# Kernel optimization log

Hardware: AMD Instinct MI355X
Metric: run time of the kernel (lower is better)

## Reference

```python
import jax, jax.numpy as jnp
import numpy as np

# Poincare ball, curvature c = 1.0 (manifold.c)
C = 1.0
SQC = 1.0  # sqrt(C)
EPS = 1e-15
BALL_EPS = 1e-5
ALPHA = 0.1  # params[0]


def _project(x):
    # clip points back inside the open ball
    norm = jnp.linalg.norm(x, axis=-1, keepdims=True)
    maxnorm = (1.0 - BALL_EPS) / SQC
    return jnp.where(norm > maxnorm, x / jnp.maximum(norm, EPS) * maxnorm, x)


def _artanh(x):
    return jnp.arctanh(jnp.clip(x, -1.0 + 1e-7, 1.0 - 1e-7))


def _lambda_x(x):
    # conformal factor lambda_x = 2 / (1 - c||x||^2)
    return 2.0 / jnp.maximum(1.0 - C * jnp.sum(x * x, axis=-1, keepdims=True), EPS)


def _mobius_scalar_mul(r, x):
    n = jnp.maximum(jnp.linalg.norm(x, axis=-1, keepdims=True), EPS)
    return jnp.tanh(r * _artanh(SQC * n)) * x / (SQC * n)


def _mobius_add(x, y):
    x2 = jnp.sum(x * x, axis=-1, keepdims=True)
    y2 = jnp.sum(y * y, axis=-1, keepdims=True)
    xy = jnp.sum(x * y, axis=-1, keepdims=True)
    num = (1.0 + 2.0 * C * xy + C * y2) * x + (1.0 - C * x2) * y
    den = 1.0 + 2.0 * C * xy + C * C * x2 * y2
    return num / jnp.maximum(den, EPS)


def _expmap0(u):
    n = jnp.maximum(jnp.linalg.norm(u, axis=-1, keepdims=True), EPS)
    return jnp.tanh(SQC * n) * u / (SQC * n)


def _mobius_matvec(W, x):
    # Mobius matrix-vector multiply: expmap0-style rescale of x @ W^T
    xn = jnp.maximum(jnp.linalg.norm(x, axis=-1, keepdims=True), EPS)
    mx = x @ W.T
    mxn = jnp.maximum(jnp.linalg.norm(mx, axis=-1, keepdims=True), EPS)
    res = jnp.tanh(mxn / xn * _artanh(SQC * xn)) * mx / (SQC * mxn)
    return _project(res)


def _clamp_abs(x, eps=1e-10):
    return jnp.where(x >= 0, jnp.maximum(x, eps), jnp.minimum(x, -eps))


def weighted_midpoint_spmm(x, src, dst, w, n):
    # gyro-midpoint of neighbors under sparse adjacency weights
    gamma = _lambda_x(x)                                   # [N,1]
    msg = (gamma * x)[src] * w[:, None]                    # [E,d] irregular gather
    num = jax.ops.segment_sum(msg, dst, num_segments=n)    # [N,d]
    den = jax.ops.segment_sum(jnp.abs(w) * (gamma[:, 0] - 1.0)[src], dst,
                              num_segments=n)[:, None]     # [N,1]
    return _project(_mobius_scalar_mul(0.5, num / _clamp_abs(den)))


def weighted_midpoint_pair(a, b, wa, wb):
    # weighted_midpoint(stack([a,b],dim=1), weights=[wa,wb], reducedim=[1])
    ga, gb = _lambda_x(a), _lambda_x(b)
    num = wa * ga * a + wb * gb * b
    den = abs(wa) * (ga - 1.0) + abs(wb) * (gb - 1.0)
    return _project(_mobius_scalar_mul(0.5, num / _clamp_abs(den)))


def setup_inputs() -> dict:
    key = jax.random.key(0)
    kx, kh, kw, kW, kb, ks, kd = jax.random.split(key, 7)
    N, D, E = 100000, 48, 1600000

    def to_ball(u):
        # squash gaussian samples well inside the Poincare ball
        n = jnp.linalg.norm(u, axis=-1, keepdims=True)
        return 0.5 * u / (1.0 + n)

    x = to_ball(jax.random.normal(kx, (N, D), dtype=jnp.float32))
    h_init = to_ball(jax.random.normal(kh, (N, D), dtype=jnp.float32))
    edge_w = jax.random.uniform(kw, (E,), dtype=jnp.float32, minval=0.01, maxval=1.0)
    W = jax.random.normal(kW, (D, D), dtype=jnp.float32) * (1.0 / np.sqrt(D))
    bias = jax.random.normal(kb, (D,), dtype=jnp.float32) * 0.01
    edge_src = jax.random.randint(ks, (E,), 0, N, dtype=jnp.int32)
    edge_dst = jax.random.randint(kd, (E,), 0, N, dtype=jnp.int32)
    return {"x": x, "h_init": h_init, "edge_w": edge_w, "W": W, "bias": bias,
            "edge_src": edge_src, "edge_dst": edge_dst}


def reference(x, h_init, edge_w, W, bias, edge_src, edge_dst):
    n = x.shape[0]
    # 1) sparse adjacency-weighted hyperbolic midpoint aggregation
    support = weighted_midpoint_spmm(x, edge_src, edge_dst, edge_w, n)
    # 2) residual midpoint with h_init, weights [1-alpha, alpha]
    support = weighted_midpoint_pair(support, h_init, 1.0 - ALPHA, ALPHA)
    # 3) Mobius linear (HyperbolicLinearFast, eval-mode dropout, no nonlin)
    h = _mobius_matvec(W, support)
    h = _project(_mobius_add(h, _expmap0(bias[None, :])))
    return h
```

## Files before the change

kernel.cpp:

```cpp
#include <hip/hip_runtime.h>
#include <math.h>

#define D  48
#define DQ 12
#define SPAN 128
#define SHIFT 7
#define PCH  8192
#define PTH  512

constexpr float F_EPS   = 1e-15f;
constexpr float MAXNORM = 1.0f - 1e-5f;

__device__ __forceinline__ float artanh_c(float x) {
    x = fminf(x, 1.0f - 1e-7f);
    x = fmaxf(x, -1.0f + 1e-7f);
    return atanhf(x);
}

__device__ __forceinline__ float clampabs(float x) {
    return (x >= 0.0f) ? fmaxf(x, 1e-10f) : fminf(x, -1e-10f);
}

__device__ __forceinline__ unsigned short f2bf(float f) {
    unsigned u = __float_as_uint(f);
    u += 0x7FFFu + ((u >> 16) & 1u);
    return (unsigned short)(u >> 16);
}

__device__ __forceinline__ float bf2f(unsigned short u) {
    return __uint_as_float(((unsigned)u) << 16);
}

__global__ void k_gamma(const float* __restrict__ x, float* __restrict__ gam,
                        int* __restrict__ ghist, int n, int nb)
{
    int i = blockIdx.x * blockDim.x + threadIdx.x;
    if (i < nb) ghist[i] = 0;
    if (i >= n) return;
    const float4* xr = reinterpret_cast<const float4*>(x) + (size_t)i * DQ;
    float s = 0.0f;
#pragma unroll
    for (int q = 0; q < DQ; ++q) {
        float4 v = xr[q];
        s += v.x * v.x + v.y * v.y + v.z * v.z + v.w * v.w;
    }
    gam[i] = 2.0f / fmaxf(1.0f - s, F_EPS);
}

__global__ __launch_bounds__(PTH) void k_hist(const int* __restrict__ dst,
                                              int* __restrict__ ghist, int E, int nb)
{
    __shared__ int h[1024];
    int t = threadIdx.x;
    for (int i = t; i < 1024; i += PTH) h[i] = 0;
    __syncthreads();
    int base = blockIdx.x * PCH;
#pragma unroll 4
    for (int k = 0; k < PCH / PTH; ++k) {
        int i = base + k * PTH + t;
        if (i < E) {
            unsigned b = ((unsigned)dst[i]) >> SHIFT;
            if (b < 1024u) atomicAdd(&h[b], 1);
        }
    }
    __syncthreads();
    for (int i = t; i < nb; i += PTH) {
        int c = h[i];
        if (c) atomicAdd(&ghist[i], c);
    }
}

__global__ __launch_bounds__(1024) void k_scanb(const int* __restrict__ ghist,
                                                int* __restrict__ gstart,
                                                int* __restrict__ gcur, int nb, int E)
{
    __shared__ int sh[1024];
    int t = threadIdx.x;
    int v = (t < nb) ? ghist[t] : 0;
    sh[t] = v;
    __syncthreads();
    for (int off = 1; off < 1024; off <<= 1) {
        int a = sh[t];
        int b = (t >= off) ? sh[t - off] : 0;
        __syncthreads();
        sh[t] = a + b;
        __syncthreads();
    }
    if (t < nb) { int s = sh[t] - v; gstart[t] = s; gcur[t] = s; }
    if (t == 0) gstart[nb] = E;
}

__global__ __launch_bounds__(PTH) void k_part(const int* __restrict__ src,
                                              const int* __restrict__ dst,
                                              const float* __restrict__ w,
                                              const float* __restrict__ gam,
                                              int* __restrict__ gcur,
                                              int2* __restrict__ seg, int E, int nb)
{
    __shared__ int hist[1024];
    __shared__ int base_[1024];
    __shared__ int lcur[1024];
    int t = threadIdx.x;
    for (int i = t; i < 1024; i += PTH) { hist[i] = 0; base_[i] = 0; lcur[i] = 0; }
    __syncthreads();
    int b0 = blockIdx.x * PCH;
#pragma unroll 4
    for (int k = 0; k < PCH / PTH; ++k) {
        int i = b0 + k * PTH + t;
        if (i < E) {
            unsigned b = ((unsigned)dst[i]) >> SHIFT;
            if (b < 1024u) atomicAdd(&hist[b], 1);
        }
    }
    __syncthreads();
    for (int i = t; i < nb; i += PTH) {
        int c = hist[i];
        if (c) base_[i] = atomicAdd(&gcur[i], c);
    }
    __syncthreads();
#pragma unroll 4
    for (int k = 0; k < PCH / PTH; ++k) {
        int i = b0 + k * PTH + t;
        if (i < E) {
            int d = dst[i];
            unsigned b = ((unsigned)d) >> SHIFT;
            if (b < 1024u) {
                int s = src[i];
                float wv = w[i];
                float g  = gam[s];
                unsigned short wb  = f2bf(wv);
                unsigned short wdb = f2bf(fabsf(wv) * (g - 1.0f));
                int pos = base_[b] + atomicAdd(&lcur[b], 1);
                if (pos >= 0 && pos < E) {
                    int2 r;
                    r.x = ((d & (SPAN - 1)) << 24) | (s & 0xFFFFFF);
                    r.y = ((unsigned)wb << 16) | wdb;
                    seg[pos] = r;
                }
            }
        }
    }
}

__global__ __launch_bounds__(256) void k_sortb(
    const int2* __restrict__ seg, const int* __restrict__ gstart,
    int* __restrict__ starts, int2* __restrict__ seg2, int n, int E)
{
    __shared__ int hist[SPAN];
    __shared__ int sb[SPAN];
    __shared__ int cur[SPAN];
    int b = blockIdx.x;
    int t = threadIdx.x;
    if (b == 0 && t == 0) starts[n] = E;
    int segL = gstart[b], segR = gstart[b + 1];
    if (segL < 0) segL = 0;
    if (segR > E) segR = E;
    if (t < SPAN) hist[t] = 0;
    __syncthreads();
    {
        int j = segL + t;
        for (; j + 768 < segR; j += 1024) {
            unsigned d0 = ((unsigned)seg[j      ].x) >> 24;
            unsigned d1 = ((unsigned)seg[j + 256].x) >> 24;
            unsigned d2 = ((unsigned)seg[j + 512].x) >> 24;
            unsigned d3 = ((unsigned)seg[j + 768].x) >> 24;
            atomicAdd(&hist[d0], 1);
            atomicAdd(&hist[d1], 1);
            atomicAdd(&hist[d2], 1);
            atomicAdd(&hist[d3], 1);
        }
        for (; j < segR; j += 256) {
            unsigned dl = ((unsigned)seg[j].x) >> 24;
            atomicAdd(&hist[dl], 1);
        }
    }
    __syncthreads();
    if (t < SPAN) sb[t] = hist[t];
    __syncthreads();
    for (int off = 1; off < SPAN; off <<= 1) {
        int a = 0;
        if (t < SPAN) { a = sb[t]; if (t >= off) a += sb[t - off]; }
        __syncthreads();
        if (t < SPAN) sb[t] = a;
        __syncthreads();
    }
    if (t < SPAN) {
        int ls = sb[t] - hist[t];
        cur[t] = segL + ls;
        int node = b * SPAN + t;
        if (node < n) starts[node] = segL + ls;
    }
    __syncthreads();
    {
        int j = segL + t;
        for (; j + 768 < segR; j += 1024) {
            int2 r0 = seg[j      ];
            int2 r1 = seg[j + 256];
            int2 r2 = seg[j + 512];
            int2 r3 = seg[j + 768];
            int p0 = atomicAdd(&cur[((unsigned)r0.x) >> 24], 1);
            int p1 = atomicAdd(&cur[((unsigned)r1.x) >> 24], 1);
            int p2 = atomicAdd(&cur[((unsigned)r2.x) >> 24], 1);
            int p3 = atomicAdd(&cur[((unsigned)r3.x) >> 24], 1);
            if (p0 >= 0 && p0 < E) seg2[p0] = make_int2(r0.x & 0xFFFFFF, r0.y);
            if (p1 >= 0 && p1 < E) seg2[p1] = make_int2(r1.x & 0xFFFFFF, r1.y);
            if (p2 >= 0 && p2 < E) seg2[p2] = make_int2(r2.x & 0xFFFFFF, r2.y);
            if (p3 >= 0 && p3 < E) seg2[p3] = make_int2(r3.x & 0xFFFFFF, r3.y);
        }
        for (; j < segR; j += 256) {
            int2 r = seg[j];
            int pos = atomicAdd(&cur[((unsigned)r.x) >> 24], 1);
            if (pos >= 0 && pos < E) seg2[pos] = make_int2(r.x & 0xFFFFFF, r.y);
        }
    }
}

__global__ __launch_bounds__(256) void k_prep(const float* __restrict__ x,
                                              const float* __restrict__ gam,
                                              ushort4* __restrict__ ybf, int n)
{
    long long t = (long long)blockIdx.x * blockDim.x + threadIdx.x;
    int node = (int)(t / DQ);
    if (node >= n) return;
    int part = (int)(t % DQ);
    float g = gam[node];
    float4 v = reinterpret_cast<const float4*>(x)[(size_t)node * DQ + part];
    ushort4 o;
    o.x = f2bf(v.x * g);
    o.y = f2bf(v.y * g);
    o.z = f2bf(v.z * g);
    o.w = f2bf(v.w * g);
    ybf[(size_t)node * DQ + part] = o;
}

__global__ __launch_bounds__(256) void k_gather(
    const ushort4* __restrict__ ybf,
    const int* __restrict__ starts,
    const int2* __restrict__ srec,
    float* __restrict__ num, float* __restrict__ den, int n, int E)
{
    long long t = (long long)blockIdx.x * blockDim.x + threadIdx.x;
    int node = (int)(t / DQ);
    if (node >= n) return;
    int part = (int)(t % DQ);
    int j0 = starts[node], j1 = starts[node + 1];
    if (j0 < 0) j0 = 0;
    if (j1 > E) j1 = E;
    float4 acc = make_float4(0.f, 0.f, 0.f, 0.f);
    float dacc = 0.f;
    int j = j0;
    for (; j + 3 < j1; j += 4) {
        int2 r0 = srec[j];
        int2 r1 = srec[j + 1];
        int2 r2 = srec[j + 2];
        int2 r3 = srec[j + 3];
        ushort4 a0 = ybf[(size_t)(r0.x) * DQ + part];
        ushort4 a1 = ybf[(size_t)(r1.x) * DQ + part];
        ushort4 a2 = ybf[(size_t)(r2.x) * DQ + part];
        ushort4 a3 = ybf[(size_t)(r3.x) * DQ + part];
        float w0 = bf2f((unsigned short)(((unsigned)r0.y) >> 16));
        float w1 = bf2f((unsigned short)(((unsigned)r1.y) >> 16));
        float w2 = bf2f((unsigned short)(((unsigned)r2.y) >> 16));
        float w3 = bf2f((unsigned short)(((unsigned)r3.y) >> 16));
        acc.x = fmaf(w0, bf2f(a0.x), acc.x);
        acc.y = fmaf(w0, bf2f(a0.y), acc.y);
        acc.z = fmaf(w0, bf2f(a0.z), acc.z);
        acc.w = fmaf(w0, bf2f(a0.w), acc.w);
        acc.x = fmaf(w1, bf2f(a1.x), acc.x);
        acc.y = fmaf(w1, bf2f(a1.y), acc.y);
        acc.z = fmaf(w1, bf2f(a1.z), acc.z);
        acc.w = fmaf(w1, bf2f(a1.w), acc.w);
        acc.x = fmaf(w2, bf2f(a2.x), acc.x);
        acc.y = fmaf(w2, bf2f(a2.y), acc.y);
        acc.z = fmaf(w2, bf2f(a2.z), acc.z);
        acc.w = fmaf(w2, bf2f(a2.w), acc.w);
        acc.x = fmaf(w3, bf2f(a3.x), acc.x);
        acc.y = fmaf(w3, bf2f(a3.y), acc.y);
        acc.z = fmaf(w3, bf2f(a3.z), acc.z);
        acc.w = fmaf(w3, bf2f(a3.w), acc.w);
        dacc += bf2f((unsigned short)(((unsigned)r0.y) & 0xFFFF))
              + bf2f((unsigned short)(((unsigned)r1.y) & 0xFFFF))
              + bf2f((unsigned short)(((unsigned)r2.y) & 0xFFFF))
              + bf2f((unsigned short)(((unsigned)r3.y) & 0xFFFF));
    }
    for (; j < j1; ++j) {
        int2 r0 = srec[j];
        ushort4 a0 = ybf[(size_t)(r0.x) * DQ + part];
        float w0 = bf2f((unsigned short)(((unsigned)r0.y) >> 16));
        acc.x = fmaf(w0, bf2f(a0.x), acc.x);
        acc.y = fmaf(w0, bf2f(a0.y), acc.y);
        acc.z = fmaf(w0, bf2f(a0.z), acc.z);
        acc.w = fmaf(w0, bf2f(a0.w), acc.w);
        dacc += bf2f((unsigned short)(((unsigned)r0.y) & 0xFFFF));
    }
    reinterpret_cast<float4*>(num)[(size_t)node * DQ + part] = acc;
    if (part == 0) den[node] = dacc;
}

__global__ void k_init_atomic(float* __restrict__ den, float* __restrict__ num, int n)
{
    int i = blockIdx.x * blockDim.x + threadIdx.x;
    if (i >= n) return;
    den[i] = 0.0f;
    float4* nr = reinterpret_cast<float4*>(num) + (size_t)i * DQ;
    float4 z = make_float4(0.f, 0.f, 0.f, 0.f);
#pragma unroll
    for (int q = 0; q < DQ; ++q) nr[q] = z;
}

__global__ void k_edge_atomic(const float* __restrict__ x, const float* __restrict__ gam,
                              const int* __restrict__ src, const int* __restrict__ dst,
                              const float* __restrict__ w,
                              float* __restrict__ num, float* __restrict__ den, int E)
{
    long long t = (long long)blockIdx.x * blockDim.x + threadIdx.x;
    int e = (int)(t / DQ);
    if (e >= E) return;
    int part = (int)(t % DQ);
    int s = src[e];
    int d = dst[e];
    float we = w[e];
    float g  = gam[s];
    float4 xv = reinterpret_cast<const float4*>(x)[(size_t)s * DQ + part];
    float c = we * g;
    float* np_ = num + (size_t)d * D + part * 4;
    atomicAdd(np_ + 0, c * xv.x);
    atomicAdd(np_ + 1, c * xv.y);
    atomicAdd(np_ + 2, c * xv.z);
    atomicAdd(np_ + 3, c * xv.w);
    if (part == 0) atomicAdd(den + d, fabsf(we) * (g - 1.0f));
}

__device__ __forceinline__ void half_mul_project(float* v)
{
    float s = 0.f;
#pragma unroll
    for (int k = 0; k < D; ++k) s += v[k] * v[k];
    float nrm = sqrtf(s);
    float ncl = fmaxf(nrm, F_EPS);
    float t   = tanhf(0.5f * artanh_c(ncl));
    float sc  = t / ncl;
    float rn  = nrm * sc;
    if (rn > MAXNORM) sc *= MAXNORM / fmaxf(rn, F_EPS);
#pragma unroll
    for (int k = 0; k < D; ++k) v[k] *= sc;
}

__global__ __launch_bounds__(256) void k_node(
    float* __restrict__ out,
    const float* __restrict__ den,
    const float* __restrict__ h_init,
    const float* __restrict__ Wm,
    const float* __restrict__ bias, int n)
{
    int i = blockIdx.x * blockDim.x + threadIdx.x;
    if (i >= n) return;

    float a[D];
    {
        const float4* nr = reinterpret_cast<const float4*>(out) + (size_t)i * DQ;
        float dinv = 1.0f / clampabs(den[i]);
#pragma unroll
        for (int q = 0; q < DQ; ++q) {
            float4 v = nr[q];
            a[q * 4 + 0] = v.x * dinv;
            a[q * 4 + 1] = v.y * dinv;
            a[q * 4 + 2] = v.z * dinv;
            a[q * 4 + 3] = v.w * dinv;
        }
    }
    half_mul_project(a);

    {
        float b[D];
        const float4* hr = reinterpret_cast<const float4*>(h_init) + (size_t)i * DQ;
#pragma unroll
        for (int q = 0; q < DQ; ++q) {
            float4 v = hr[q];
            b[q * 4 + 0] = v.x; b[q * 4 + 1] = v.y;
            b[q * 4 + 2] = v.z; b[q * 4 + 3] = v.w;
        }
        float sa = 0.f, sb = 0.f;
#pragma unroll
        for (int k = 0; k < D; ++k) { sa += a[k] * a[k]; sb += b[k] * b[k]; }
        float ga = 2.0f / fmaxf(1.0f - sa, F_EPS);
        float gb = 2.0f / fmaxf(1.0f - sb, F_EPS);
        const float wa = 0.9f, wb = 0.1f;
        float dinv = 1.0f / clampabs(wa * (ga - 1.0f) + wb * (gb - 1.0f));
        float ca = wa * ga * dinv, cb = wb * gb * dinv;
#pragma unroll
        for (int k = 0; k < D; ++k) a[k] = ca * a[k] + cb * b[k];
        half_mul_project(a);
    }

    float sa2 = 0.f;
#pragma unroll
    for (int k = 0; k < D; ++k) sa2 += a[k] * a[k];
    float xn = fmaxf(sqrtf(sa2), F_EPS);

    float smx = 0.f, xyr = 0.f;
#pragma unroll 4
    for (int j = 0; j < D; ++j) {
        float acc = 0.f;
#pragma unroll
        for (int k = 0; k < D; ++k) acc = fmaf(Wm[j * D + k], a[k], acc);
        smx += acc * acc;
        xyr = fmaf(acc, bias[j], xyr);
    }
    float mxnr = sqrtf(smx);
    float mxn = fmaxf(mxnr, F_EPS);
    float tt = tanhf((mxn / xn) * artanh_c(xn));
    float sc = tt / mxn;
    float rn = mxnr * sc;
    if (rn > MAXNORM) sc *= MAXNORM / fmaxf(rn, F_EPS);

    float bn2 = 0.f;
#pragma unroll
    for (int k = 0; k < D; ++k) bn2 = fmaf(bias[k], bias[k], bn2);
    float bn  = fmaxf(sqrtf(bn2), F_EPS);
    float ebs = tanhf(bn) / bn;
    float y2  = ebs * ebs * bn2;

    float x2 = sc * sc * smx;
    float xy = sc * ebs * xyr;
    float c1 = 1.0f + 2.0f * xy + y2;
    float c2 = 1.0f - x2;
    float dn3 = 1.0f / fmaxf(1.0f + 2.0f * xy + x2 * y2, F_EPS);

    float s3 = dn3 * dn3 * (c1 * c1 * sc * sc * smx
                            + 2.0f * c1 * c2 * sc * ebs * xyr
                            + c2 * c2 * ebs * ebs * bn2);
    float nrm3 = sqrtf(s3);
    float fp = (nrm3 > MAXNORM) ? (MAXNORM / fmaxf(nrm3, F_EPS)) : 1.0f;

    float CA = c1 * sc * dn3 * fp;
    float CB = c2 * ebs * dn3 * fp;

    float4* orow = reinterpret_cast<float4*>(out) + (size_t)i * DQ;
    for (int q = 0; q < DQ; ++q) {
        float e[4];
#pragma unroll
        for (int jj = 0; jj < 4; ++jj) {
            int j = q * 4 + jj;
            float acc = 0.f;
#pragma unroll
            for (int k = 0; k < D; ++k) acc = fmaf(Wm[j * D + k], a[k], acc);
            e[jj] = fmaf(CA, acc, CB * bias[j]);
        }
        float4 v;
        v.x = e[0]; v.y = e[1]; v.z = e[2]; v.w = e[3];
        orow[q] = v;
    }
}

extern "C" void kernel_launch(void* const* d_in, const int* in_sizes, int n_in,
                              void* d_out, int out_size, void* d_ws, size_t ws_size,
                              hipStream_t stream)
{
    const float* x      = (const float*)d_in[0];
    const float* h_init = (const float*)d_in[1];
    const float* edge_w = (const float*)d_in[2];
    const float* W      = (const float*)d_in[3];
    const float* bias   = (const float*)d_in[4];
    const int*   esrc   = (const int*)d_in[5];
    const int*   edst   = (const int*)d_in[6];
    float* out = (float*)d_out;

    int n = in_sizes[0] / D;
    int E = in_sizes[2];
    int nb = (n + SPAN - 1) >> SHIFT;

    char* p = (char*)d_ws;
    float* gam    = (float*)p;             p += (size_t)n * 4;
    float* den    = (float*)p;             p += (size_t)n * 4;
    int*   ghist  = (int*)p;               p += (size_t)nb * 4;
    int*   gstart = (int*)p;               p += (size_t)(nb + 1) * 4;
    int*   gcur   = (int*)p;               p += (size_t)nb * 4;
    int*   starts = (int*)p;               p += (size_t)(n + 1) * 4;
    p = (char*)(((uintptr_t)p + 15) & ~(uintptr_t)15);
    int2*  seg    = (int2*)p;              p += (size_t)E * 8;
    int2*  seg2   = (int2*)p;              p += (size_t)E * 8;
    size_t need1 = (size_t)(p - (char*)d_ws);
    ushort4* ybf = (ushort4*)seg;
    bool ybf_fits = ((size_t)E * 8 >= (size_t)n * D * 2);

    k_gamma<<<(n + 255) / 256, 256, 0, stream>>>(x, gam, ghist, n, nb);

    bool shape_ok = (nb <= 1024) && (n < (1 << 24));
    if (shape_ok && ybf_fits && need1 <= ws_size) {
        int pb = (E + PCH - 1) / PCH;
        k_hist<<<pb, PTH, 0, stream>>>(edst, ghist, E, nb);
        k_scanb<<<1, 1024, 0, stream>>>(ghist, gstart, gcur, nb, E);
        k_part<<<pb, PTH, 0, stream>>>(esrc, edst, edge_w, gam, gcur, seg, E, nb);
        k_sortb<<<nb, 256, 0, stream>>>(seg, gstart, starts, seg2, n, E);
        long long tot = (long long)n * DQ;
        int gg = (int)((tot + 255) / 256);
        k_prep<<<gg, 256, 0, stream>>>(x, gam, ybf, n);
        k_gather<<<gg, 256, 0, stream>>>(ybf, starts, seg2, out, den, n, E);
    } else {
        k_init_atomic<<<(n + 255) / 256, 256, 0, stream>>>(den, out, n);
        long long tot = (long long)E * DQ;
        k_edge_atomic<<<(int)((tot + 255) / 256), 256, 0, stream>>>(x, gam, esrc, edst, edge_w, out, den, E);
    }

    k_node<<<(n + 255) / 256, 256, 0, stream>>>(out, den, h_init, W, bias, n);
}
```

Before: 164.3 us.

## Split per-node epilogue across 16-lane groups with shared-memory weight matrix

The node kernel previously used one thread per node, holding a 48-float vector in registers and computing the 48x48 matvec twice from global memory. It now assigns 16 lanes per node, each holding three components. Norms are reduced with subgroup shuffles, W and bias are staged in padded LDS, and the matvec result is computed once and reused for the output. This targets register pressure, redundant matvec work and uncoalesced per-thread row access, at the cost of more blocks and extra W staging per block.

```diff
diff --git a/kernel.cpp b/kernel.cpp
--- a/kernel.cpp
+++ b/kernel.cpp
@@ -7,6 +7,8 @@
 #define SHIFT 7
 #define PCH  8192
 #define PTH  512
+#define NPB  16
+#define WSTR 52
 
 constexpr float F_EPS   = 1e-15f;
 constexpr float MAXNORM = 1.0f - 1e-5f;
@@ -331,21 +333,6 @@
     if (part == 0) atomicAdd(den + d, fabsf(we) * (g - 1.0f));
 }
 
-__device__ __forceinline__ void half_mul_project(float* v)
-{
-    float s = 0.f;
-#pragma unroll
-    for (int k = 0; k < D; ++k) s += v[k] * v[k];
-    float nrm = sqrtf(s);
-    float ncl = fmaxf(nrm, F_EPS);
-    float t   = tanhf(0.5f * artanh_c(ncl));
-    float sc  = t / ncl;
-    float rn  = nrm * sc;
-    if (rn > MAXNORM) sc *= MAXNORM / fmaxf(rn, F_EPS);
-#pragma unroll
-    for (int k = 0; k < D; ++k) v[k] *= sc;
-}
-
 __global__ __launch_bounds__(256) void k_node(
     float* __restrict__ out,
     const float* __restrict__ den,
@@ -353,60 +340,99 @@
     const float* __restrict__ Wm,
     const float* __restrict__ bias, int n)
 {
-    int i = blockIdx.x * blockDim.x + threadIdx.x;
-    if (i >= n) return;
-
-    float a[D];
+    __shared__ float Ws[D * WSTR];
+    __shared__ float bs[D];
+    __shared__ float aLds[NPB][D];
+    int t = threadIdx.x;
+    for (int k = t; k < D * D; k += 256) Ws[(k / D) * WSTR + (k % D)] = Wm[k];
+    if (t < D) bs[t] = bias[t];
+    __syncthreads();
+
+    int grp = t >> 4;
+    int lane = t & 15;
+    int i = blockIdx.x * NPB + grp;
+    bool act = (i < n);
+
+    auto gsum = [](float v) {
+        v += __shfl_xor(v, 1, 16);
+        v += __shfl_xor(v, 2, 16);
+        v += __shfl_xor(v, 4, 16);
+        v += __shfl_xor(v, 8, 16);
+        return v;
+    };
+
+    float a0 = 0.f, a1 = 0.f, a2 = 0.f;
+    if (act) {
+        float dinv = 1.0f / clampabs(den[i]);
+        const float* nr = out + (size_t)i * D;
+        a0 = nr[lane] * dinv;
+        a1 = nr[lane + 16] * dinv;
+        a2 = nr[lane + 32] * dinv;
+    }
     {
-        const float4* nr = reinterpret_cast<const float4*>(out) + (size_t)i * DQ;
-        float dinv = 1.0f / clampabs(den[i]);
-#pragma unroll
-        for (int q = 0; q < DQ; ++q) {
-            float4 v = nr[q];
-            a[q * 4 + 0] = v.x * dinv;
-            a[q * 4 + 1] = v.y * dinv;
-            a[q * 4 + 2] = v.z * dinv;
-            a[q * 4 + 3] = v.w * dinv;
-        }
-    }
-    half_mul_project(a);
+        float s = gsum(a0 * a0 + a1 * a1 + a2 * a2);
+        float nrm = sqrtf(s);
+        float ncl = fmaxf(nrm, F_EPS);
+        float tt = tanhf(0.5f * artanh_c(ncl));
+        float sc = tt / ncl;
+        float rn = nrm * sc;
+        if (rn > MAXNORM) sc *= MAXNORM / fmaxf(rn, F_EPS);
+        a0 *= sc; a1 *= sc; a2 *= sc;
+    }
 
     {
-        float b[D];
-        const float4* hr = reinterpret_cast<const float4*>(h_init) + (size_t)i * DQ;
-#pragma unroll
-        for (int q = 0; q < DQ; ++q) {
-            float4 v = hr[q];
-            b[q * 4 + 0] = v.x; b[q * 4 + 1] = v.y;
-            b[q * 4 + 2] = v.z; b[q * 4 + 3] = v.w;
-        }
-        float sa = 0.f, sb = 0.f;
-#pragma unroll
-        for (int k = 0; k < D; ++k) { sa += a[k] * a[k]; sb += b[k] * b[k]; }
+        float b0 = 0.f, b1 = 0.f, b2 = 0.f;
+        if (act) {
+            const float* hr = h_init + (size_t)i * D;
+            b0 = hr[lane];
+            b1 = hr[lane + 16];
+            b2 = hr[lane + 32];
+        }
+        float sa = gsum(a0 * a0 + a1 * a1 + a2 * a2);
+        float sb = gsum(b0 * b0 + b1 * b1 + b2 * b2);
         float ga = 2.0f / fmaxf(1.0f - sa, F_EPS);
         float gb = 2.0f / fmaxf(1.0f - sb, F_EPS);
         const float wa = 0.9f, wb = 0.1f;
         float dinv = 1.0f / clampabs(wa * (ga - 1.0f) + wb * (gb - 1.0f));
         float ca = wa * ga * dinv, cb = wb * gb * dinv;
+        a0 = ca * a0 + cb * b0;
+        a1 = ca * a1 + cb * b1;
+        a2 = ca * a2 + cb * b2;
+        float s = gsum(a0 * a0 + a1 * a1 + a2 * a2);
+        float nrm = sqrtf(s);
+        float ncl = fmaxf(nrm, F_EPS);
+        float tt = tanhf(0.5f * artanh_c(ncl));
+        float sc = tt / ncl;
+        float rn = nrm * sc;
+        if (rn > MAXNORM) sc *= MAXNORM / fmaxf(rn, F_EPS);
+        a0 *= sc; a1 *= sc; a2 *= sc;
+    }
+
+    aLds[grp][lane]      = a0;
+    aLds[grp][lane + 16] = a1;
+    aLds[grp][lane + 32] = a2;
+    __syncthreads();
+
+    float sa2 = gsum(a0 * a0 + a1 * a1 + a2 * a2);
+    float xn = fmaxf(sqrtf(sa2), F_EPS);
+
+    const float* av = aLds[grp];
+    const float* w0 = &Ws[lane * WSTR];
+    const float* w1 = &Ws[(lane + 16) * WSTR];
+    const float* w2 = &Ws[(lane + 32) * WSTR];
+    float acc0 = 0.f, acc1 = 0.f, acc2 = 0.f;
 #pragma unroll
-        for (int k = 0; k < D; ++k) a[k] = ca * a[k] + cb * b[k];
-        half_mul_project(a);
-    }
-
-    float sa2 = 0.f;
-#pragma unroll
-    for (int k = 0; k < D; ++k) sa2 += a[k] * a[k];
-    float xn = fmaxf(sqrtf(sa2), F_EPS);
-
-    float smx = 0.f, xyr = 0.f;
-#pragma unroll 4
-    for (int j = 0; j < D; ++j) {
-        float acc = 0.f;
-#pragma unroll
-        for (int k = 0; k < D; ++k) acc = fmaf(Wm[j * D + k], a[k], acc);
-        smx += acc * acc;
-        xyr = fmaf(acc, bias[j], xyr);
-    }
+    for (int k = 0; k < D; ++k) {
+        float ak = av[k];
+        acc0 = fmaf(w0[k], ak, acc0);
+        acc1 = fmaf(w1[k], ak, acc1);
+        acc2 = fmaf(w2[k], ak, acc2);
+    }
+    float bl0 = bs[lane], bl1 = bs[lane + 16], bl2 = bs[lane + 32];
+    float smx = gsum(acc0 * acc0 + acc1 * acc1 + acc2 * acc2);
+    float xyr = gsum(acc0 * bl0 + acc1 * bl1 + acc2 * bl2);
+    float bn2 = gsum(bl0 * bl0 + bl1 * bl1 + bl2 * bl2);
+
     float mxnr = sqrtf(smx);
     float mxn = fmaxf(mxnr, F_EPS);
     float tt = tanhf((mxn / xn) * artanh_c(xn));
@@ -414,9 +440,6 @@
     float rn = mxnr * sc;
     if (rn > MAXNORM) sc *= MAXNORM / fmaxf(rn, F_EPS);
 
-    float bn2 = 0.f;
-#pragma unroll
-    for (int k = 0; k < D; ++k) bn2 = fmaf(bias[k], bias[k], bn2);
     float bn  = fmaxf(sqrtf(bn2), F_EPS);
     float ebs = tanhf(bn) / bn;
     float y2  = ebs * ebs * bn2;
@@ -436,20 +459,11 @@
     float CA = c1 * sc * dn3 * fp;
     float CB = c2 * ebs * dn3 * fp;
 
-    float4* orow = reinterpret_cast<float4*>(out) + (size_t)i * DQ;
-    for (int q = 0; q < DQ; ++q) {
-        float e[4];
-#pragma unroll
-        for (int jj = 0; jj < 4; ++jj) {
-            int j = q * 4 + jj;
-            float acc = 0.f;
-#pragma unroll
-            for (int k = 0; k < D; ++k) acc = fmaf(Wm[j * D + k], a[k], acc);
-            e[jj] = fmaf(CA, acc, CB * bias[j]);
-        }
-        float4 v;
-        v.x = e[0]; v.y = e[1]; v.z = e[2]; v.w = e[3];
-        orow[q] = v;
+    if (act) {
+        float* orow = out + (size_t)i * D;
+        orow[lane]      = fmaf(CA, acc0, CB * bl0);
+        orow[lane + 16] = fmaf(CA, acc1, CB * bl1);
+        orow[lane + 32] = fmaf(CA, acc2, CB * bl2);
     }
 }
 
@@ -503,5 +517,5 @@
         k_edge_atomic<<<(int)((tot + 255) / 256), 256, 0, stream>>>(x, gam, esrc, edst, edge_w, out, den, E);
     }
 
-    k_node<<<(n + 255) / 256, 256, 0, stream>>>(out, den, h_init, W, bias, n);
-}
+    k_node<<<(n + NPB - 1) / NPB, 256, 0, stream>>>(out, den, h_init, W, bias, n);
+}
```

Measured after the change: 156.7 us. 1.05x faster.
